# Performance work log

Measured on AMD Instinct MI355X. Metric: run time of the kernel, lower is better.

## Reference

```python
import jax, jax.numpy as jnp
import numpy as np

N_NODES, N_EDGES, H = 50000, 800000, 96


def setup_inputs() -> dict:
    key = jax.random.key(0)
    ks = jax.random.split(key, 8)
    s = 1.0 / np.sqrt(H)  # xavier-ish scale
    g = lambda k, shape, sc=1.0: jax.random.normal(k, shape, jnp.float32) * sc
    return {
        "x": g(ks[0], (N_NODES, H)),
        "conn": g(ks[1], (N_EDGES, H)),
        "edge_index": jax.random.randint(ks[2], (2, N_EDGES), 0, N_NODES),  # row0=dst, row1=src
        "qkv_w": g(ks[3], (3 * H, H), s),
        "qkv_b": jnp.zeros((3 * H,), jnp.float32),
        "e_w": g(ks[4], (2 * H, H), s),
        "e_b": jnp.zeros((2 * H,), jnp.float32),
        "conn_lin_w": g(ks[5], (H, H), s),
        "conn_lin_b": jnp.zeros((H,), jnp.float32),
        "nodelin_w": g(ks[6], (H, H), s),
        "nodelin_b": jnp.zeros((H,), jnp.float32),
        "ln_h_g": jnp.ones((H,), jnp.float32),
        "ln_h_b": jnp.zeros((H,), jnp.float32),
        "ln_e_g": jnp.ones((H,), jnp.float32),
        "ln_e_b": jnp.zeros((H,), jnp.float32),
    }


def _layernorm(v, g, b, eps=1e-5):
    mu = v.mean(-1, keepdims=True)
    var = ((v - mu) ** 2).mean(-1, keepdims=True)
    return (v - mu) * jax.lax.rsqrt(var + eps) * g + b


def reference(x, conn, edge_index, qkv_w, qkv_b, e_w, e_b, conn_lin_w, conn_lin_b,
              nodelin_w, nodelin_b, ln_h_g, ln_h_b, ln_e_g, ln_e_b):
    n = x.shape[0]
    # packed QKV projection (attn_dim*attn_heads == hidden_dim)
    qkv = x @ qkv_w.T + qkv_b                      # [N, 3H]
    Qh, Kh, Vh = jnp.split(qkv, 3, axis=-1)        # each [N, H]
    # edge feature projection -> (Ew, Eb)
    Eh = (conn @ e_w.T + e_b).reshape(conn.shape[0], 2, H)  # [E, 2, H]
    Ew, Eb = Eh[:, 0, :], Eh[:, 1, :]
    dst, src = edge_index[0], edge_index[1]
    # gather -> elementwise signed-sqrt -> activation
    c1 = (Qh[dst] + Kh[src]) * Ew                  # [E, H]
    c2 = jnp.sign(c1) * jnp.sqrt(jnp.abs(c1))      # == sqrt(relu(c1)) - sqrt(relu(-c1))
    conn_out = jax.nn.relu(c2 + Eb)                # [E, H]
    # scatter-reduce (agg='add')
    agg = jax.ops.segment_sum(Vh[src], dst, num_segments=n)            # [N, H]
    eagg = jax.ops.segment_sum(conn_out, dst, num_segments=n)          # [N, H]
    eagg = eagg @ conn_lin_w.T + conn_lin_b
    h = (agg + eagg) @ nodelin_w.T + nodelin_b     # nodelin (dropout p=0)
    h = x + h                                      # residual
    e = conn + conn_out
    return _layernorm(h, ln_h_g, ln_h_b), _layernorm(e, ln_e_g, ln_e_b)
```

## Files before the change

kernel.cpp:

```cpp
#include <hip/hip_runtime.h>
#include <math.h>

#define N_NODES 50000
#define N_EDGES 800000
#define H 96
#define QKV_N 288

#define NPB1 32
#define NPB3 4
#define NPB3B 8
#define NPA 32

typedef __attribute__((ext_vector_type(8))) short short8;
typedef __attribute__((ext_vector_type(4))) float f32x4;

__device__ __forceinline__ short f2bf(float f) {
    union { float f; unsigned u; } v; v.f = f;
    unsigned r = v.u + 0x7FFFu + ((v.u >> 16) & 1u);
    return (short)(r >> 16);
}
__device__ __forceinline__ float bf2f(unsigned short h) {
    union { unsigned u; float f; } v; v.u = ((unsigned)h) << 16;
    return v.f;
}

__device__ __forceinline__ void ld_frag_split(const float* __restrict__ p,
                                              short8& hi, short8& lo) {
    float4 a = *(const float4*)p;
    float4 b = *(const float4*)(p + 4);
    float f[8] = {a.x, a.y, a.z, a.w, b.x, b.y, b.z, b.w};
    #pragma unroll
    for (int j = 0; j < 8; ++j) {
        union { float f; unsigned u; } v; v.f = f[j];
        hi[j] = (short)(v.u >> 16);
        union { unsigned u; float f; } h; h.u = v.u & 0xFFFF0000u;
        union { float f; unsigned u; } l; l.f = f[j] - h.f;
        lo[j] = (short)(l.u >> 16);
    }
}

__global__ __launch_bounds__(QKV_N) void qkv_kernel(
    const float* __restrict__ x, const float* __restrict__ qw,
    const float* __restrict__ qb, float* __restrict__ qkv,
    unsigned short* __restrict__ vbf)
{
    __shared__ __align__(16) float xs[H];
    const int t = threadIdx.x;

    float w[H];
    #pragma unroll
    for (int k4 = 0; k4 < H; k4 += 4) {
        float4 v = *(const float4*)(qw + (size_t)t * H + k4);
        w[k4] = v.x; w[k4 + 1] = v.y; w[k4 + 2] = v.z; w[k4 + 3] = v.w;
    }
    const float bias = qb[t];

    const int n0 = blockIdx.x * NPB1;
    for (int nn = 0; nn < NPB1; ++nn) {
        const int node = n0 + nn;
        if (node >= N_NODES) break;
        __syncthreads();
        if (t < H) xs[t] = x[(size_t)node * H + t];
        __syncthreads();
        float acc = bias;
        #pragma unroll
        for (int k4 = 0; k4 < H; k4 += 4) {
            float4 c = *(const float4*)(xs + k4);
            acc += c.x * w[k4] + c.y * w[k4 + 1] + c.z * w[k4 + 2] + c.w * w[k4 + 3];
        }
        qkv[(size_t)node * QKV_N + t] = acc;
        if (vbf && t >= 2 * H)
            vbf[(size_t)node * H + (t - 2 * H)] = (unsigned short)f2bf(acc);
    }
}

__global__ __launch_bounds__(256) void hist_kernel(const int* __restrict__ eidx,
                                                   int* __restrict__ hist) {
    const int e = blockIdx.x * 256 + threadIdx.x;
    if (e < N_EDGES) atomicAdd(&hist[eidx[e]], 1);
}

#define SCAN_CH 49
__global__ __launch_bounds__(1024) void scan_kernel(int* __restrict__ hist,
                                                    int* __restrict__ rowptr) {
    __shared__ int sums[1024];
    const int t = threadIdx.x;
    const int st = t * SCAN_CH;
    int loc = 0;
    for (int k = 0; k < SCAN_CH; ++k) {
        const int i = st + k;
        if (i < N_NODES) loc += hist[i];
    }
    sums[t] = loc;
    __syncthreads();
    for (int off = 1; off < 1024; off <<= 1) {
        int add = (t >= off) ? sums[t - off] : 0;
        __syncthreads();
        sums[t] += add;
        __syncthreads();
    }
    int run = sums[t] - loc;
    for (int k = 0; k < SCAN_CH; ++k) {
        const int i = st + k;
        if (i < N_NODES) {
            const int v = hist[i];
            rowptr[i] = run;
            hist[i]   = run;
            run += v;
        }
    }
    if (t == 1023) rowptr[N_NODES] = run;
}

__global__ __launch_bounds__(256) void scatter_kernel(const int* __restrict__ eidx,
                                                      int* __restrict__ cursor,
                                                      int* __restrict__ bucket,
                                                      int* __restrict__ bsrc,
                                                      int* __restrict__ dstof) {
    const int e = blockIdx.x * 256 + threadIdx.x;
    if (e < N_EDGES) {
        const int dst = eidx[e];
        const int src = eidx[N_EDGES + e];
        const int pos = atomicAdd(&cursor[dst], 1);
        bucket[pos] = e;
        bsrc[pos]   = src;
        if (dstof) dstof[pos] = dst;
    }
}

#define TILE_E 64
#define EH_LD 196

template <bool COBF>
__global__ __launch_bounds__(256) void edge_kernel(
    const float* __restrict__ conn, const int* __restrict__ eidx,
    const float* __restrict__ qkv,
    const float* __restrict__ ew, const float* __restrict__ eb,
    unsigned short* __restrict__ co_bf, float* __restrict__ out_e)
{
    __shared__ __align__(16) float eh[TILE_E * EH_LD];

    const int t    = threadIdx.x;
    const int wave = t >> 6;
    const int lane = t & 63;
    const int lr   = lane & 15;
    const int lg16 = lane >> 4;

    short8 bwh[3][3], bwl[3][3];
    #pragma unroll
    for (int f = 0; f < 3; ++f) {
        const int tcol = 16 * (3 * wave + f) + lr;
        #pragma unroll
        for (int kc = 0; kc < 3; ++kc)
            ld_frag_split(ew + (size_t)tcol * H + 32 * kc + 8 * lg16,
                          bwh[f][kc], bwl[f][kc]);
    }

    const int e0 = blockIdx.x * TILE_E;

    f32x4 acc[4][3];
    #pragma unroll
    for (int mt = 0; mt < 4; ++mt)
        #pragma unroll
        for (int f = 0; f < 3; ++f)
            acc[mt][f] = (f32x4){0.f, 0.f, 0.f, 0.f};

    #pragma unroll
    for (int mt = 0; mt < 4; ++mt) {
        const int erow = e0 + 16 * mt + lr;
        short8 ah[3], al[3];
        #pragma unroll
        for (int kc = 0; kc < 3; ++kc)
            ld_frag_split(conn + (size_t)erow * H + 32 * kc + 8 * lg16,
                          ah[kc], al[kc]);
        #pragma unroll
        for (int f = 0; f < 3; ++f) {
            #pragma unroll
            for (int kc = 0; kc < 3; ++kc) {
                acc[mt][f] = __builtin_amdgcn_mfma_f32_16x16x32_bf16(
                                 ah[kc], bwl[f][kc], acc[mt][f], 0, 0, 0);
                acc[mt][f] = __builtin_amdgcn_mfma_f32_16x16x32_bf16(
                                 al[kc], bwh[f][kc], acc[mt][f], 0, 0, 0);
                acc[mt][f] = __builtin_amdgcn_mfma_f32_16x16x32_bf16(
                                 ah[kc], bwh[f][kc], acc[mt][f], 0, 0, 0);
            }
        }
    }

    #pragma unroll
    for (int mt = 0; mt < 4; ++mt) {
        #pragma unroll
        for (int f = 0; f < 3; ++f) {
            const int col = 16 * (3 * wave + f) + lr;
            const float bias = eb[col];
            #pragma unroll
            for (int r = 0; r < 4; ++r) {
                const int row = 16 * mt + 4 * lg16 + r;
                eh[row * EH_LD + col] = acc[mt][f][r] + bias;
            }
        }
    }
    __syncthreads();

    const int e_loc = t >> 2;
    const int q4    = t & 3;
    const int e     = e0 + e_loc;
    const int dst   = eidx[e];
    const int src   = eidx[N_EDGES + e];
    const float4* qQ4 = (const float4*)(qkv + (size_t)dst * QKV_N) + 6 * q4;
    const float4* qK4 = (const float4*)(qkv + (size_t)src * QKV_N + H) + 6 * q4;
    float4*          oe4 = (float4*)(out_e + (size_t)e * H) + 6 * q4;
    unsigned short*  cb  = COBF ? (co_bf + (size_t)e * H + 24 * q4) : nullptr;
    const float*  ehr = &eh[e_loc * EH_LD + 24 * q4];

    #pragma unroll
    for (int i = 0; i < 6; ++i) {
        const float4 q  = qQ4[i];
        const float4 k  = qK4[i];
        const float4 w4 = *(const float4*)(ehr + 4 * i);
        const float4 b4 = *(const float4*)(ehr + 4 * i + H);
        float4 co4;
        #pragma unroll
        for (int jj = 0; jj < 4; ++jj) {
            const float c1 = (q[jj] + k[jj]) * w4[jj];
            const float c2 = copysignf(sqrtf(fabsf(c1)), c1);
            co4[jj] = fmaxf(c2 + b4[jj], 0.f);
        }
        if (COBF) {
            ushort4 pk;
            pk.x = (unsigned short)f2bf(co4[0]);
            pk.y = (unsigned short)f2bf(co4[1]);
            pk.z = (unsigned short)f2bf(co4[2]);
            pk.w = (unsigned short)f2bf(co4[3]);
            *(ushort4*)(cb + 4 * i) = pk;
        } else {
            oe4[i] = co4;
        }
    }
}

template <bool COBF>
__global__ __launch_bounds__(256) void eln_kernel(
    const float* __restrict__ conn, const unsigned short* __restrict__ co_bf,
    const float* __restrict__ ln_g, const float* __restrict__ ln_b,
    float* __restrict__ out_e)
{
    const int tt   = blockIdx.x * 256 + threadIdx.x;
    const size_t e = (size_t)(tt >> 2);
    const int q4   = tt & 3;
    const float4* cn4 = (const float4*)(conn + e * H) + 6 * q4;
    float4*       oe4 = (float4*)(out_e + e * H) + 6 * q4;
    const float4* g4  = (const float4*)ln_g + 6 * q4;
    const float4* b4  = (const float4*)ln_b + 6 * q4;

    float4 v[6];
    float s = 0.f, s2 = 0.f;
    if (COBF) {
        const short8* cb8 = (const short8*)(co_bf + e * H + 24 * q4);
        #pragma unroll
        for (int j = 0; j < 3; ++j) {
            const short8 c8 = cb8[j];
            const float4 cA = cn4[2 * j];
            const float4 cB = cn4[2 * j + 1];
            #pragma unroll
            for (int k = 0; k < 4; ++k) {
                const float a = cA[k] + bf2f((unsigned short)c8[k]);
                const float b = cB[k] + bf2f((unsigned short)c8[4 + k]);
                v[2 * j][k] = a; v[2 * j + 1][k] = b;
                s += a + b; s2 += a * a + b * b;
            }
        }
    } else {
        #pragma unroll
        for (int i = 0; i < 6; ++i) {
            const float4 c = cn4[i];
            const float4 o = oe4[i];
            float4 val;
            #pragma unroll
            for (int jj = 0; jj < 4; ++jj) {
                val[jj] = c[jj] + o[jj];
                s += val[jj]; s2 += val[jj] * val[jj];
            }
            v[i] = val;
        }
    }
    s  += __shfl_xor(s, 1);  s  += __shfl_xor(s, 2);
    s2 += __shfl_xor(s2, 1); s2 += __shfl_xor(s2, 2);
    const float mean = s * (1.f / H);
    const float var  = s2 * (1.f / H) - mean * mean;
    const float rs   = rsqrtf(var + 1e-5f);
    #pragma unroll
    for (int i = 0; i < 6; ++i) {
        const float4 g = g4[i], b = b4[i];
        float4 o;
        #pragma unroll
        for (int jj = 0; jj < 4; ++jj)
            o[jj] = (v[i][jj] - mean) * rs * g[jj] + b[jj];
        oe4[i] = o;
    }
}

template <bool VBF, bool COBF>
__global__ __launch_bounds__(256) void agg_kernel(
    const float* __restrict__ qkv, const unsigned short* __restrict__ vbf,
    const float* __restrict__ co, const unsigned short* __restrict__ co_bf,
    const int* __restrict__ rowptr, const int* __restrict__ bucket,
    const int* __restrict__ bsrc, const int* __restrict__ dstof,
    float* __restrict__ agg, float* __restrict__ eagg)
{
    __shared__ float accA[NPA][H];
    __shared__ float accE[NPA][H];
    const int t = threadIdx.x;

    for (int i = t; i < NPA * H; i += 256) {
        ((float*)accA)[i] = 0.f;
        ((float*)accE)[i] = 0.f;
    }
    __syncthreads();

    const int n0   = blockIdx.x * NPA;
    const int nend = (n0 + NPA < N_NODES) ? (n0 + NPA) : N_NODES;
    const int P0 = rowptr[n0], P1 = rowptr[nend];
    const int count = P1 - P0;
    const int quad = t >> 2, q4 = t & 3;
    const int len  = (count + 63) >> 6;
    int p    = P0 + quad * len;
    int pend = p + len; if (pend > P1) pend = P1;

    float4 va[6], ve[6];
    #pragma unroll
    for (int i = 0; i < 6; ++i) { va[i] = (float4){0,0,0,0}; ve[i] = (float4){0,0,0,0}; }
    int cur = -1;

    for (; p < pend; ++p) {
        const int slot = dstof[p] - n0;
        if (slot != cur) {
            if (cur >= 0) {
                #pragma unroll
                for (int i = 0; i < 6; ++i)
                    #pragma unroll
                    for (int jj = 0; jj < 4; ++jj) {
                        atomicAdd(&accA[cur][24 * q4 + 4 * i + jj], va[i][jj]);
                        atomicAdd(&accE[cur][24 * q4 + 4 * i + jj], ve[i][jj]);
                    }
                #pragma unroll
                for (int i = 0; i < 6; ++i) { va[i] = (float4){0,0,0,0}; ve[i] = (float4){0,0,0,0}; }
            }
            cur = slot;
        }
        const int e  = bucket[p];
        const int sv = bsrc[p];
        if (VBF) {
            const short8* vb8 = (const short8*)(vbf + (size_t)sv * H + 24 * q4);
            #pragma unroll
            for (int j = 0; j < 3; ++j) {
                const short8 v8 = vb8[j];
                #pragma unroll
                for (int k = 0; k < 8; ++k) {
                    const int idx = 8 * j + k;
                    va[idx >> 2][idx & 3] += bf2f((unsigned short)v8[k]);
                }
            }
        } else {
            const float4* v4 = (const float4*)(qkv + (size_t)sv * QKV_N + 2 * H) + 6 * q4;
            #pragma unroll
            for (int i = 0; i < 6; ++i) {
                const float4 a = v4[i];
                #pragma unroll
                for (int jj = 0; jj < 4; ++jj) va[i][jj] += a[jj];
            }
        }
        if (COBF) {
            const short8* cb8 = (const short8*)(co_bf + (size_t)e * H + 24 * q4);
            #pragma unroll
            for (int j = 0; j < 3; ++j) {
                const short8 c8 = cb8[j];
                #pragma unroll
                for (int k = 0; k < 8; ++k) {
                    const int idx = 8 * j + k;
                    ve[idx >> 2][idx & 3] += bf2f((unsigned short)c8[k]);
                }
            }
        } else {
            const float4* c4 = (const float4*)(co + (size_t)e * H) + 6 * q4;
            #pragma unroll
            for (int i = 0; i < 6; ++i) {
                const float4 b = c4[i];
                #pragma unroll
                for (int jj = 0; jj < 4; ++jj) ve[i][jj] += b[jj];
            }
        }
    }
    if (cur >= 0) {
        #pragma unroll
        for (int i = 0; i < 6; ++i)
            #pragma unroll
            for (int jj = 0; jj < 4; ++jj) {
                atomicAdd(&accA[cur][24 * q4 + 4 * i + jj], va[i][jj]);
                atomicAdd(&accE[cur][24 * q4 + 4 * i + jj], ve[i][jj]);
            }
    }
    __syncthreads();

    const int nloc = nend - n0;
    for (int i = t; i < nloc * H; i += 256) {
        const int r = i / H, c = i - r * H;
        agg [(size_t)(n0 + r) * H + c] = accA[r][c];
        eagg[(size_t)(n0 + r) * H + c] = accE[r][c];
    }
}

__global__ __launch_bounds__(192) void node_kernel_big(
    const float* __restrict__ x,
    const float* __restrict__ agg, const float* __restrict__ eagg,
    const float* __restrict__ clw, const float* __restrict__ clb,
    const float* __restrict__ nlw, const float* __restrict__ nlb,
    const float* __restrict__ ln_g, const float* __restrict__ ln_b,
    float* __restrict__ out_h)
{
    __shared__ __align__(16) float ga[H];
    __shared__ __align__(16) float sa[H];
    __shared__ float red0[H], red1[H];
    const int t = threadIdx.x;

    float w[H];
    {
        const float* wsrc = (t < H) ? (clw + (size_t)t * H) : (nlw + (size_t)(t - H) * H);
        #pragma unroll
        for (int k4 = 0; k4 < H; k4 += 4) {
            float4 v = *(const float4*)(wsrc + k4);
            w[k4] = v.x; w[k4 + 1] = v.y; w[k4 + 2] = v.z; w[k4 + 3] = v.w;
        }
    }
    const float bias = (t < H) ? clb[t] : nlb[t - H];
    const float lg = (t >= H) ? ln_g[t - H] : 0.f;
    const float lb = (t >= H) ? ln_b[t - H] : 0.f;

    const int n0 = blockIdx.x * NPB3B;
    for (int nn = 0; nn < NPB3B; ++nn) {
        const int node = n0 + nn;
        if (node >= N_NODES) break;
        __syncthreads();
        if (t < H)       ga[t]     = eagg[(size_t)node * H + t];
        else             sa[t - H] = agg[(size_t)node * H + (t - H)];
        __syncthreads();

        if (t < H) {
            float acc = bias;
            #pragma unroll
            for (int k4 = 0; k4 < H; k4 += 4) {
                float4 c = *(const float4*)(ga + k4);
                acc += c.x * w[k4] + c.y * w[k4 + 1] + c.z * w[k4 + 2] + c.w * w[k4 + 3];
            }
            sa[t] += acc;
        }
        __syncthreads();

        float val = 0.f;
        if (t >= H) {
            const int tt = t - H;
            float acc = bias;
            #pragma unroll
            for (int k4 = 0; k4 < H; k4 += 4) {
                float4 c = *(const float4*)(sa + k4);
                acc += c.x * w[k4] + c.y * w[k4 + 1] + c.z * w[k4 + 2] + c.w * w[k4 + 3];
            }
            val = acc + x[(size_t)node * H + tt];
            red0[tt] = val;
            red1[tt] = val * val;
        }
        __syncthreads();
        if (t < 32) { red0[t] += red0[t + 64]; red1[t] += red1[t + 64]; }
        __syncthreads();
        for (int s = 32; s > 0; s >>= 1) {
            if (t < s) { red0[t] += red0[t + s]; red1[t] += red1[t + s]; }
            __syncthreads();
        }
        if (t >= H) {
            const float mean = red0[0] * (1.f / H);
            const float var  = red1[0] * (1.f / H) - mean * mean;
            const float r    = rsqrtf(var + 1e-5f);
            out_h[(size_t)node * H + (t - H)] = (val - mean) * r * lg + lb;
        }
    }
}

__global__ __launch_bounds__(192) void node_kernel(
    const float* __restrict__ x, const float* __restrict__ qkv,
    const float* __restrict__ co_f32,
    const int* __restrict__ rowptr, const int* __restrict__ bucket,
    const int* __restrict__ bsrc,
    const float* __restrict__ clw, const float* __restrict__ clb,
    const float* __restrict__ nlw, const float* __restrict__ nlb,
    const float* __restrict__ ln_g, const float* __restrict__ ln_b,
    float* __restrict__ out_h)
{
    __shared__ __align__(16) float ga[H];
    __shared__ __align__(16) float sa[H];
    __shared__ float pa2[192], pe2[192];
    __shared__ float red0[H], red1[H];
    const int t = threadIdx.x;
    const int col = (t < H) ? t : (t - H);
    const int par = (t < H) ? 0 : 1;

    float w[H];
    {
        const float* wsrc = (t < H) ? (clw + (size_t)t * H) : (nlw + (size_t)(t - H) * H);
        #pragma unroll
        for (int k4 = 0; k4 < H; k4 += 4) {
            float4 v = *(const float4*)(wsrc + k4);
            w[k4] = v.x; w[k4 + 1] = v.y; w[k4 + 2] = v.z; w[k4 + 3] = v.w;
        }
    }
    const float bias = (t < H) ? clb[t] : nlb[t - H];
    const float lg = (t >= H) ? ln_g[t - H] : 0.f;
    const float lb = (t >= H) ? ln_b[t - H] : 0.f;

    const int n0 = blockIdx.x * NPB3;
    for (int nn = 0; nn < NPB3; ++nn) {
        const int node = n0 + nn;
        if (node >= N_NODES) break;
        const int r0 = rowptr[node], r1 = rowptr[node + 1];

        float pa = 0.f, pe = 0.f;
        for (int j = r0 + par; j < r1; j += 2) {
            const int ee = bucket[j];
            const int sv = bsrc[j];
            pa += qkv[(size_t)sv * QKV_N + 2 * H + col];
            pe += co_f32[(size_t)ee * H + col];
        }
        __syncthreads();
        pa2[t] = pa; pe2[t] = pe;
        __syncthreads();
        if (t < H) ga[t]      = pe2[t] + pe2[t + H];
        else       sa[t - H]  = pa2[t - H] + pa2[t];
        __syncthreads();

        if (t < H) {
            float acc = bias;
            #pragma unroll
            for (int k4 = 0; k4 < H; k4 += 4) {
                float4 c = *(const float4*)(ga + k4);
                acc += c.x * w[k4] + c.y * w[k4 + 1] + c.z * w[k4 + 2] + c.w * w[k4 + 3];
            }
            sa[t] += acc;
        }
        __syncthreads();

        float val = 0.f;
        if (t >= H) {
            const int tt = t - H;
            float acc = bias;
            #pragma unroll
            for (int k4 = 0; k4 < H; k4 += 4) {
                float4 c = *(const float4*)(sa + k4);
                acc += c.x * w[k4] + c.y * w[k4 + 1] + c.z * w[k4 + 2] + c.w * w[k4 + 3];
            }
            val = acc + x[(size_t)node * H + tt];
            red0[tt] = val;
            red1[tt] = val * val;
        }
        __syncthreads();
        if (t < 32) { red0[t] += red0[t + 64]; red1[t] += red1[t + 64]; }
        __syncthreads();
        for (int s = 32; s > 0; s >>= 1) {
            if (t < s) { red0[t] += red0[t + s]; red1[t] += red1[t + s]; }
            __syncthreads();
        }
        if (t >= H) {
            const float mean = red0[0] * (1.f / H);
            const float var  = red1[0] * (1.f / H) - mean * mean;
            const float r    = rsqrtf(var + 1e-5f);
            out_h[(size_t)node * H + (t - H)] = (val - mean) * r * lg + lb;
        }
    }
}

extern "C" void kernel_launch(void* const* d_in, const int* in_sizes, int n_in,
                              void* d_out, int out_size, void* d_ws, size_t ws_size,
                              hipStream_t stream) {
    const float* x      = (const float*)d_in[0];
    const float* conn   = (const float*)d_in[1];
    const int*   eidx   = (const int*)  d_in[2];
    const float* qkv_w  = (const float*)d_in[3];
    const float* qkv_b  = (const float*)d_in[4];
    const float* e_w    = (const float*)d_in[5];
    const float* e_b    = (const float*)d_in[6];
    const float* clw    = (const float*)d_in[7];
    const float* clb    = (const float*)d_in[8];
    const float* nlw    = (const float*)d_in[9];
    const float* nlb    = (const float*)d_in[10];
    const float* ln_h_g = (const float*)d_in[11];
    const float* ln_h_b = (const float*)d_in[12];
    const float* ln_e_g = (const float*)d_in[13];
    const float* ln_e_b = (const float*)d_in[14];

    float* out_h = (float*)d_out;
    float* out_e = out_h + (size_t)N_NODES * H;

    char* base = (char*)d_ws;
    float* qkv = (float*)base;
    size_t off = (size_t)N_NODES * QKV_N * sizeof(float);
    int* rowptr = (int*)(base + off); off += (size_t)(N_NODES + 1) * 4;
    int* hist   = (int*)(base + off); off += (size_t)N_NODES * 4;
    int* bucket = (int*)(base + off); off += (size_t)N_EDGES * 4;
    int* bsrc   = (int*)(base + off); off += (size_t)N_EDGES * 4;
    int*   dstof = (int*)(base + off);  off += (size_t)N_EDGES * 4;
    float* agg   = (float*)(base + off); off += (size_t)N_NODES * H * 4;
    float* eagg  = (float*)(base + off); off += (size_t)N_NODES * H * 4;
    unsigned short* vbf = (unsigned short*)(base + off);
    off += (size_t)N_NODES * H * 2;
    const size_t need_B = off;
    unsigned short* cobf = (unsigned short*)(base + off);
    off += (size_t)N_EDGES * H * 2;
    const size_t need_A = off;

    const bool A = ws_size >= need_A;
    const bool B = !A && ws_size >= need_B;

    hipMemsetAsync(hist, 0, (size_t)N_NODES * 4, stream);

    qkv_kernel    <<<(N_NODES + NPB1 - 1) / NPB1, QKV_N, 0, stream>>>(
        x, qkv_w, qkv_b, qkv, (A || B) ? vbf : nullptr);
    hist_kernel   <<<(N_EDGES + 255) / 256, 256, 0, stream>>>(eidx, hist);
    scan_kernel   <<<1, 1024, 0, stream>>>(hist, rowptr);
    scatter_kernel<<<(N_EDGES + 255) / 256, 256, 0, stream>>>(eidx, hist, bucket, bsrc,
                                                              (A || B) ? dstof : nullptr);

    if (A) {
        edge_kernel<true><<<N_EDGES / TILE_E, 256, 0, stream>>>(
            conn, eidx, qkv, e_w, e_b, cobf, out_e);
        agg_kernel<true, true><<<(N_NODES + NPA - 1) / NPA, 256, 0, stream>>>(
            qkv, vbf, out_e, cobf, rowptr, bucket, bsrc, dstof, agg, eagg);
        node_kernel_big<<<(N_NODES + NPB3B - 1) / NPB3B, 192, 0, stream>>>(
            x, agg, eagg, clw, clb, nlw, nlb, ln_h_g, ln_h_b, out_h);
        eln_kernel<true><<<(N_EDGES * 4) / 256, 256, 0, stream>>>(
            conn, cobf, ln_e_g, ln_e_b, out_e);
    } else if (B) {
        edge_kernel<false><<<N_EDGES / TILE_E, 256, 0, stream>>>(
            conn, eidx, qkv, e_w, e_b, nullptr, out_e);
        agg_kernel<true, false><<<(N_NODES + NPA - 1) / NPA, 256, 0, stream>>>(
            qkv, vbf, out_e, nullptr, rowptr, bucket, bsrc, dstof, agg, eagg);
        node_kernel_big<<<(N_NODES + NPB3B - 1) / NPB3B, 192, 0, stream>>>(
            x, agg, eagg, clw, clb, nlw, nlb, ln_h_g, ln_h_b, out_h);
        eln_kernel<false><<<(N_EDGES * 4) / 256, 256, 0, stream>>>(
            conn, nullptr, ln_e_g, ln_e_b, out_e);
    } else {
        edge_kernel<false><<<N_EDGES / TILE_E, 256, 0, stream>>>(
            conn, eidx, qkv, e_w, e_b, nullptr, out_e);
        node_kernel<<<(N_NODES + NPB3 - 1) / NPB3, 192, 0, stream>>>(
            x, qkv, out_e, rowptr, bucket, bsrc,
            clw, clb, nlw, nlb, ln_h_g, ln_h_b, out_h);
        eln_kernel<false><<<(N_EDGES * 4) / 256, 256, 0, stream>>>(
            conn, nullptr, ln_e_g, ln_e_b, out_e);
    }
}
```

Measured before the change: 1.225 ms.

## Fuse edge LayerNorm into aggregation kernel on the bf16 conn_out path

On the default workspace path, the aggregation kernel now reads the bf16 conn_out once, adds it into the per-node accumulator, and in the same pass adds conn, computes the edge LayerNorm and writes out_e. This removes the separate eln_kernel launch and its second read of conn_out. In exchange, conn reads and out_e writes now follow the dst-sorted bucket order, so they are scattered rather than streamed. The agg kernel also carries more registers and work per edge, which may lower occupancy.

```diff
diff --git a/kernel.cpp b/kernel.cpp
--- a/kernel.cpp
+++ b/kernel.cpp
@@ -239,9 +239,8 @@
     }
 }
 
-template <bool COBF>
 __global__ __launch_bounds__(256) void eln_kernel(
-    const float* __restrict__ conn, const unsigned short* __restrict__ co_bf,
+    const float* __restrict__ conn,
     const float* __restrict__ ln_g, const float* __restrict__ ln_b,
     float* __restrict__ out_e)
 {
@@ -255,34 +254,17 @@
 
     float4 v[6];
     float s = 0.f, s2 = 0.f;
-    if (COBF) {
-        const short8* cb8 = (const short8*)(co_bf + e * H + 24 * q4);
-        #pragma unroll
-        for (int j = 0; j < 3; ++j) {
-            const short8 c8 = cb8[j];
-            const float4 cA = cn4[2 * j];
-            const float4 cB = cn4[2 * j + 1];
-            #pragma unroll
-            for (int k = 0; k < 4; ++k) {
-                const float a = cA[k] + bf2f((unsigned short)c8[k]);
-                const float b = cB[k] + bf2f((unsigned short)c8[4 + k]);
-                v[2 * j][k] = a; v[2 * j + 1][k] = b;
-                s += a + b; s2 += a * a + b * b;
-            }
-        }
-    } else {
-        #pragma unroll
-        for (int i = 0; i < 6; ++i) {
-            const float4 c = cn4[i];
-            const float4 o = oe4[i];
-            float4 val;
-            #pragma unroll
-            for (int jj = 0; jj < 4; ++jj) {
-                val[jj] = c[jj] + o[jj];
-                s += val[jj]; s2 += val[jj] * val[jj];
-            }
-            v[i] = val;
-        }
+    #pragma unroll
+    for (int i = 0; i < 6; ++i) {
+        const float4 c = cn4[i];
+        const float4 o = oe4[i];
+        float4 val;
+        #pragma unroll
+        for (int jj = 0; jj < 4; ++jj) {
+            val[jj] = c[jj] + o[jj];
+            s += val[jj]; s2 += val[jj] * val[jj];
+        }
+        v[i] = val;
     }
     s  += __shfl_xor(s, 1);  s  += __shfl_xor(s, 2);
     s2 += __shfl_xor(s2, 1); s2 += __shfl_xor(s2, 2);
@@ -304,6 +286,9 @@
 __global__ __launch_bounds__(256) void agg_kernel(
     const float* __restrict__ qkv, const unsigned short* __restrict__ vbf,
     const float* __restrict__ co, const unsigned short* __restrict__ co_bf,
+    const float* __restrict__ conn,
+    const float* __restrict__ ln_g, const float* __restrict__ ln_b,
+    float* __restrict__ out_e,
     const int* __restrict__ rowptr, const int* __restrict__ bucket,
     const int* __restrict__ bsrc, const int* __restrict__ dstof,
     float* __restrict__ agg, float* __restrict__ eagg)
@@ -372,14 +357,39 @@
         }
         if (COBF) {
             const short8* cb8 = (const short8*)(co_bf + (size_t)e * H + 24 * q4);
+            short8 c8[3];
+            c8[0] = cb8[0]; c8[1] = cb8[1]; c8[2] = cb8[2];
+            const float4* cn4 = (const float4*)(conn + (size_t)e * H) + 6 * q4;
+            float4 v_s[6];
+            float s = 0.f, s2 = 0.f;
             #pragma unroll
             for (int j = 0; j < 3; ++j) {
-                const short8 c8 = cb8[j];
                 #pragma unroll
                 for (int k = 0; k < 8; ++k) {
                     const int idx = 8 * j + k;
-                    ve[idx >> 2][idx & 3] += bf2f((unsigned short)c8[k]);
+                    const float cov = bf2f((unsigned short)c8[j][k]);
+                    ve[idx >> 2][idx & 3] += cov;
+                    const float val = cn4[idx >> 2][idx & 3] + cov;
+                    v_s[idx >> 2][idx & 3] = val;
+                    s += val; s2 += val * val;
                 }
+            }
+            s  += __shfl_xor(s, 1);  s  += __shfl_xor(s, 2);
+            s2 += __shfl_xor(s2, 1); s2 += __shfl_xor(s2, 2);
+            const float mean = s * (1.f / H);
+            const float var  = s2 * (1.f / H) - mean * mean;
+            const float rs   = rsqrtf(var + 1e-5f);
+            float4* oe4 = (float4*)(out_e + (size_t)e * H) + 6 * q4;
+            const float4* g4 = (const float4*)ln_g + 6 * q4;
+            const float4* b4 = (const float4*)ln_b + 6 * q4;
+            #pragma unroll
+            for (int i = 0; i < 6; ++i) {
+                const float4 g = g4[i], b = b4[i];
+                float4 o;
+                #pragma unroll
+                for (int jj = 0; jj < 4; ++jj)
+                    o[jj] = (v_s[i][jj] - mean) * rs * g[jj] + b[jj];
+                oe4[i] = o;
             }
         } else {
             const float4* c4 = (const float4*)(co + (size_t)e * H) + 6 * q4;
@@ -631,27 +641,27 @@
         edge_kernel<true><<<N_EDGES / TILE_E, 256, 0, stream>>>(
             conn, eidx, qkv, e_w, e_b, cobf, out_e);
         agg_kernel<true, true><<<(N_NODES + NPA - 1) / NPA, 256, 0, stream>>>(
-            qkv, vbf, out_e, cobf, rowptr, bucket, bsrc, dstof, agg, eagg);
+            qkv, vbf, nullptr, cobf, conn, ln_e_g, ln_e_b, out_e,
+            rowptr, bucket, bsrc, dstof, agg, eagg);
         node_kernel_big<<<(N_NODES + NPB3B - 1) / NPB3B, 192, 0, stream>>>(
             x, agg, eagg, clw, clb, nlw, nlb, ln_h_g, ln_h_b, out_h);
-        eln_kernel<true><<<(N_EDGES * 4) / 256, 256, 0, stream>>>(
-            conn, cobf, ln_e_g, ln_e_b, out_e);
     } else if (B) {
         edge_kernel<false><<<N_EDGES / TILE_E, 256, 0, stream>>>(
             conn, eidx, qkv, e_w, e_b, nullptr, out_e);
         agg_kernel<true, false><<<(N_NODES + NPA - 1) / NPA, 256, 0, stream>>>(
-            qkv, vbf, out_e, nullptr, rowptr, bucket, bsrc, dstof, agg, eagg);
+            qkv, vbf, out_e, nullptr, nullptr, nullptr, nullptr, nullptr,
+            rowptr, bucket, bsrc, dstof, agg, eagg);
         node_kernel_big<<<(N_NODES + NPB3B - 1) / NPB3B, 192, 0, stream>>>(
             x, agg, eagg, clw, clb, nlw, nlb, ln_h_g, ln_h_b, out_h);
-        eln_kernel<false><<<(N_EDGES * 4) / 256, 256, 0, stream>>>(
-            conn, nullptr, ln_e_g, ln_e_b, out_e);
+        eln_kernel<<<(N_EDGES * 4) / 256, 256, 0, stream>>>(
+            conn, ln_e_g, ln_e_b, out_e);
     } else {
         edge_kernel<false><<<N_EDGES / TILE_E, 256, 0, stream>>>(
             conn, eidx, qkv, e_w, e_b, nullptr, out_e);
         node_kernel<<<(N_NODES + NPB3 - 1) / NPB3, 192, 0, stream>>>(
             x, qkv, out_e, rowptr, bucket, bsrc,
             clw, clb, nlw, nlb, ln_h_g, ln_h_b, out_h);
-        eln_kernel<false><<<(N_EDGES * 4) / 256, 256, 0, stream>>>(
-            conn, nullptr, ln_e_g, ln_e_b, out_e);
-    }
-}
+        eln_kernel<<<(N_EDGES * 4) / 256, 256, 0, stream>>>(
+            conn, ln_e_g, ln_e_b, out_e);
+    }
+}
```

Measured after the change: 1.196 ms (median of 2 runs). -2.4%, faster.
